# Kernel optimization log

Measured on AMD Instinct MI355X. Metric: run time of the kernel, lower is better.

## Reference

```python
import jax, jax.numpy as jnp
import numpy as np

B, C_IN, C_OUT, H, W, K = 8, 32, 32, 96, 96, 5


def setup_inputs() -> dict:
    key = jax.random.key(0)
    k1, k2 = jax.random.split(key)
    f = jax.random.normal(k1, (B, C_IN, H, W), dtype=jnp.float32)
    # xavier_uniform-style init for the structuring element h
    fan_in = C_IN * K * K
    fan_out = C_OUT * K * K
    bound = float(np.sqrt(6.0 / (fan_in + fan_out)))
    h = jax.random.uniform(k2, (C_OUT, C_IN, K, K), dtype=jnp.float32,
                           minval=-bound, maxval=bound)
    return {"f": f, "h": h}


def reference(f, h):
    """Morphological max-plus dilation with 'same' padding.

    out[b,o,y,x] = max_{c,i,j} f[b,c,y+i-p, x+j-p] + h[o,c,i,j]
    """
    b, c, hh, ww = f.shape
    o, _, k, _ = h.shape
    p = k // 2
    neg = -jnp.finfo(f.dtype).max / 2
    fp = jnp.pad(f, ((0, 0), (0, 0), (p, p), (p, p)), constant_values=neg)
    out = jnp.full((b, o, hh, ww), neg, dtype=f.dtype)
    for i in range(k):          # fixed small kernel loop (k*k = 25 taps)
        for j in range(k):
            sl = fp[:, :, i:i + hh, j:j + ww]              # (B, C, H, W)
            w_ij = h[:, :, i, j]                            # (O, C)
            # max-plus over input channels: (B,1,C,H,W) + (O,C,1,1)
            cand = jnp.max(sl[:, None] + w_ij[None, :, :, None, None], axis=2)
            out = jnp.maximum(out, cand)
    return out
```

## Files before the change

kernel.cpp:

```cpp
#include <hip/hip_runtime.h>


#define B_ 8
#define C_ 32
#define O_ 32
#define H_ 96
#define W_ 96
#define K_ 5
#define KK_ (K_ * K_)
#define NCP_ (C_ / 2)

#define TX_ 24
#define RT_ 8
#define CS_ 2
#define TY_ (RT_ * CS_)
#define NT_ (TX_ * TY_)
#define XR_ 4
#define OB_ 2
#define NOG_ (O_ / OB_)
#define CPG_ (NCP_ / CS_)

#define PH_ 100
#define PW_ 104
#define PLSZ_ (PH_ * PW_)
#define FPAD_BYTES ((size_t)B_ * NCP_ * PLSZ_ * 4)

#define HBLK_ 128
#define HPH_ 16
#define HPACK_DW (NOG_ * NCP_ * HBLK_)

#define SCALE_ 2048.0f
#define INVSCALE_ (1.0f / 2048.0f)
#define NEGQ_ (-30000)
#define NEGPACK_ 0x8AD08AD0u

typedef int sv8 __attribute__((ext_vector_type(8)));
typedef int sv2 __attribute__((ext_vector_type(2)));
typedef unsigned uv4 __attribute__((ext_vector_type(4)));

static __device__ __forceinline__ int q16(float v) {
    int q = __float2int_rn(v * SCALE_);
    q = (q < -32768) ? -32768 : q;
    q = (q > 32767) ? 32767 : q;
    return q;
}
static __device__ __forceinline__ unsigned packq(int lo, int hi) {
    return (unsigned)(lo & 0xffff) | ((unsigned)hi << 16);
}

static __device__ __forceinline__ void pk_addmax_s(int& acc, int fv, int hs) {
    int t;
    asm("v_pk_add_i16 %0, %1, %2" : "=v"(t) : "v"(fv), "s"(hs));
    asm("v_pk_max_i16 %0, %1, %2" : "=v"(acc) : "v"(acc), "v"(t));
}

static __device__ __forceinline__ int getwin(uv4 a, uv4 b, int d) {
    if (d == 0) return (int)a[0];
    if (d == 1) return (int)a[1];
    if (d == 2) return (int)a[2];
    if (d == 3) return (int)a[3];
    if (d == 4) return (int)b[0];
    if (d == 5) return (int)b[1];
    if (d == 6) return (int)b[2];
    return (int)b[3];
}

static __device__ __forceinline__ void compute_phase(int (&acc)[OB_][XR_],
        uv4 wa, uv4 wb, sv8 c0, sv2 c1) {
#pragma unroll
    for (int j = 0; j < K_; ++j) {
        const int h0 = (j * 2 < 8) ? c0[j * 2] : c1[j * 2 - 8];
        const int h1 = (j * 2 + 1 < 8) ? c0[j * 2 + 1] : c1[j * 2 + 1 - 8];
#pragma unroll
        for (int xx = 0; xx < XR_; ++xx) {
            int fv = getwin(wa, wb, xx + j);
            pk_addmax_s(acc[0][xx], fv, h0);
            pk_addmax_s(acc[1][xx], fv, h1);
        }
    }
}

#define HLOADM(B0, B1, HP, O0S, O1S)                                   \
    asm volatile("s_load_dwordx8 %0, %2, " O0S "\n\t"                  \
                 "s_load_dwordx2 %1, %2, " O1S                         \
                 : "=s"(B0), "=s"(B1) : "s"(HP))

#define WLOADM(SA, SB, PTR, O0S, O1S)                                  \
    asm volatile("global_load_dwordx4 %0, %2, off offset:" O0S "\n\t"  \
                 "global_load_dwordx4 %1, %2, off offset:" O1S         \
                 : "=v"(SA), "=v"(SB) : "v"(PTR))

#define PHASE(CH0, CH1, NH0, NH1, NHP, HO0, HO1, CW, NW, NPTR, WO0, WO1) \
    do {                                                                  \
        asm volatile("s_waitcnt lgkmcnt(0)" : "+s"(CH0), "+s"(CH1));      \
        HLOADM(NH0, NH1, NHP, HO0, HO1);                                  \
        WLOADM(NW[0], NW[1], NPTR, WO0, WO1);                             \
        asm volatile("s_waitcnt vmcnt(2)" : "+v"(CW[0]), "+v"(CW[1]));    \
        compute_phase(acc, CW[0], CW[1], CH0, CH1);                       \
    } while (0)

__global__ __launch_bounds__(256)
void prep_kernel(const float* __restrict__ f, const float* __restrict__ h,
                 unsigned* __restrict__ fpad, unsigned* __restrict__ hpack) {
    const int bz = blockIdx.z;
    if (bz < B_) {
        const int idx = blockIdx.x * 256 + threadIdx.x;
        const int cp = blockIdx.y;
        if (idx >= PLSZ_) return;
        const int row = idx / PW_;
        const int col = idx - row * PW_;
        const int y = row - 2;
        const int x = col - 2;
        unsigned pk = NEGPACK_;
        if ((unsigned)y < H_ && (unsigned)x < W_) {
            float v0 = f[((size_t)(bz * C_ + 2 * cp)     * H_ + y) * W_ + x];
            float v1 = f[((size_t)(bz * C_ + 2 * cp + 1) * H_ + y) * W_ + x];
            pk = packq(q16(v0), q16(v1));
        }
        fpad[(size_t)(bz * NCP_ + cp) * PLSZ_ + idx] = pk;
    } else {
        const int t = (blockIdx.y * gridDim.x + blockIdx.x) * 256 + threadIdx.x;
        if (t >= NOG_ * NCP_ * KK_ * OB_) return;
        const int og = t / (NCP_ * KK_ * OB_);
        int r  = t - og * (NCP_ * KK_ * OB_);
        const int cp = r / (KK_ * OB_);
        r -= cp * (KK_ * OB_);
        const int ij = r / OB_;
        const int o  = r - ij * OB_;
        const int p  = ij / K_;
        const int jj = ij - p * K_;
        float a0 = h[((size_t)(og * OB_ + o) * C_ + 2 * cp)     * KK_ + ij];
        float a1 = h[((size_t)(og * OB_ + o) * C_ + 2 * cp + 1) * KK_ + ij];
        hpack[(size_t)(og * NCP_ + cp) * HBLK_ + p * HPH_ + jj * OB_ + o] =
            packq(q16(a0), q16(a1));
    }
}

__global__ __launch_bounds__(NT_, 7)
void dilate_main(const unsigned* __restrict__ fpad,
                 const unsigned* __restrict__ hpack,
                 float* __restrict__ out) {
    const int tx  = threadIdx.x;
    const int ty  = threadIdx.y;
    const int ry  = ty & (RT_ - 1);
    const int g   = ty >> 3;
    const int gu  = __builtin_amdgcn_readfirstlane(g);

    const int ytile = blockIdx.x;
    const int og    = blockIdx.y;
    const int b     = blockIdx.z;
    const int y0 = ytile * RT_;
    const int o0 = og * OB_;
    const int x0 = XR_ * tx;
    const int yb = y0 + ry;

    __shared__ unsigned short comb[OB_ * XR_][RT_ * TX_];

    int acc[OB_][XR_];
#pragma unroll
    for (int o = 0; o < OB_; ++o)
#pragma unroll
        for (int xx = 0; xx < XR_; ++xx) acc[o][xx] = (int)NEGPACK_;

    const int cp0v = g * CPG_;
    const int cp0s = gu * CPG_;
    const unsigned* hpb = hpack + (size_t)(og * NCP_ + cp0s) * HBLK_;
    const unsigned* pvb = fpad + (size_t)(b * NCP_ + cp0v) * PLSZ_ + yb * PW_ + x0;

    sv8 hA0; sv2 hA1;
    sv8 hB0; sv2 hB1;
    uv4 winA[2], winB[2];

    HLOADM(hA0, hA1, hpb, "0x0", "0x20");
    WLOADM(winA[0], winA[1], pvb, "0", "16");

#pragma unroll 1
    for (int cpi = 0; cpi < CPG_; cpi += 2) {
        const unsigned* hb0 = hpb + (size_t)cpi * HBLK_;
        const unsigned* hb1 = hb0 + HBLK_;
        const unsigned* hb2 = (cpi + 2 < CPG_) ? hb1 + HBLK_ : hb1;
        const unsigned* pv0 = pvb + (size_t)cpi * PLSZ_;
        const unsigned* pv1 = pv0 + PLSZ_;
        const unsigned* pv2 = (cpi + 2 < CPG_) ? pv1 + PLSZ_ : pv1;

        PHASE(hA0,hA1, hB0,hB1, hb0, "0x40","0x60",   winA, winB, pv0, "416","432");
        PHASE(hB0,hB1, hA0,hA1, hb0, "0x80","0xa0",   winB, winA, pv0, "832","848");
        PHASE(hA0,hA1, hB0,hB1, hb0, "0xc0","0xe0",   winA, winB, pv0, "1248","1264");
        PHASE(hB0,hB1, hA0,hA1, hb0, "0x100","0x120", winB, winA, pv0, "1664","1680");
        PHASE(hA0,hA1, hB0,hB1, hb1, "0x0","0x20",    winA, winB, pv1, "0","16");
        PHASE(hB0,hB1, hA0,hA1, hb1, "0x40","0x60",   winB, winA, pv1, "416","432");
        PHASE(hA0,hA1, hB0,hB1, hb1, "0x80","0xa0",   winA, winB, pv1, "832","848");
        PHASE(hB0,hB1, hA0,hA1, hb1, "0xc0","0xe0",   winB, winA, pv1, "1248","1264");
        PHASE(hA0,hA1, hB0,hB1, hb1, "0x100","0x120", winA, winB, pv1, "1664","1680");
        PHASE(hB0,hB1, hA0,hA1, hb2, "0x0","0x20",    winB, winA, pv2, "0","16");
    }

    asm volatile("s_waitcnt vmcnt(0) lgkmcnt(0)"
                 : "+v"(winA[0]), "+v"(winA[1]), "+s"(hA0), "+s"(hA1));

    short red[OB_][XR_];
#pragma unroll
    for (int o = 0; o < OB_; ++o)
#pragma unroll
        for (int xx = 0; xx < XR_; ++xx) {
            short a = (short)(acc[o][xx] & 0xffff);
            short b2 = (short)(((unsigned)acc[o][xx]) >> 16);
            red[o][xx] = (a > b2) ? a : b2;
        }

    const int t192 = ry * TX_ + tx;
    if (g == 1) {
#pragma unroll
        for (int o = 0; o < OB_; ++o)
#pragma unroll
            for (int xx = 0; xx < XR_; ++xx)
                comb[o * XR_ + xx][t192] = (unsigned short)red[o][xx];
    }
    __syncthreads();
    if (g == 0) {
        const int y = yb;
#pragma unroll
        for (int o = 0; o < OB_; ++o) {
            float r[XR_];
#pragma unroll
            for (int xx = 0; xx < XR_; ++xx) {
                short m  = red[o][xx];
                short v0 = (short)comb[o * XR_ + xx][t192];
                m = (v0 > m) ? v0 : m;
                r[xx] = (float)m * INVSCALE_;
            }
            float4 v = make_float4(r[0], r[1], r[2], r[3]);
            *(float4*)&out[(((size_t)b * O_ + (o0 + o)) * H_ + y) * W_ + x0] = v;
        }
    }
}

__global__ __launch_bounds__(256)
void dilate_naive(const float* __restrict__ f, const float* __restrict__ h,
                  float* __restrict__ out) {
    const int idx = blockIdx.x * 256 + threadIdx.x;
    if (idx >= B_ * O_ * H_ * W_) return;
    const int x = idx % W_;
    const int y = (idx / W_) % H_;
    const int o = (idx / (W_ * H_)) % O_;
    const int b = idx / (W_ * H_ * O_);
    float m = -3.0e38f;
    for (int c = 0; c < C_; ++c)
        for (int i = 0; i < K_; ++i)
            for (int j = 0; j < K_; ++j) {
                int yy = y + i - 2, xc = x + j - 2;
                if ((unsigned)yy < H_ && (unsigned)xc < W_) {
                    float v = f[((size_t)(b * C_ + c) * H_ + yy) * W_ + xc] +
                              h[((size_t)o * C_ + c) * KK_ + i * K_ + j];
                    m = fmaxf(m, v);
                }
            }
    out[idx] = m;
}

extern "C" void kernel_launch(void* const* d_in, const int* in_sizes, int n_in,
                              void* d_out, int out_size, void* d_ws, size_t ws_size,
                              hipStream_t stream) {
    const float* f = (const float*)d_in[0];
    const float* h = (const float*)d_in[1];
    float* out = (float*)d_out;

    const size_t need = FPAD_BYTES + (size_t)HPACK_DW * 4;
    if (ws_size >= need) {
        unsigned* fpad  = (unsigned*)d_ws;
        unsigned* hpack = (unsigned*)((char*)d_ws + FPAD_BYTES);
        dim3 pgrid((PLSZ_ + 255) / 256, NCP_, B_ + 1);
        hipLaunchKernelGGL(prep_kernel, pgrid, dim3(256), 0, stream,
                           f, h, fpad, hpack);
        dim3 mgrid(H_ / RT_, NOG_, B_);
        dim3 mblock(TX_, TY_);
        hipLaunchKernelGGL(dilate_main, mgrid, mblock, 0, stream,
                           fpad, hpack, out);
    } else {
        hipLaunchKernelGGL(dilate_naive,
                           dim3((B_ * O_ * H_ * W_ + 255) / 256), dim3(256),
                           0, stream, f, h, out);
    }
}
```

Measured before the change: 134.7 us.

## Stage padded input row slabs through LDS with double buffering

Instead of each thread loading its 5-row input window straight from global memory per tap row, the block cooperatively loads a 12-row slab per channel pair into shared memory. The next slab is fetched while the current one is computed, and threads read their windows from LDS. This cuts redundant global/L2 traffic from overlapping rows across threads. In exchange it adds LDS usage, a __syncthreads per channel pair, and LDS-read latency that may hurt the 7-waves occupancy target.

```diff
diff --git a/kernel.cpp b/kernel.cpp
--- a/kernel.cpp
+++ b/kernel.cpp
@@ -31,8 +31,9 @@
 
 #define SCALE_ 2048.0f
 #define INVSCALE_ (1.0f / 2048.0f)
-#define NEGQ_ (-30000)
 #define NEGPACK_ 0x8AD08AD0u
+
+#define SLAB_UV4 320
 
 typedef int sv8 __attribute__((ext_vector_type(8)));
 typedef int sv2 __attribute__((ext_vector_type(2)));
@@ -85,18 +86,37 @@
                  "s_load_dwordx2 %1, %2, " O1S                         \
                  : "=s"(B0), "=s"(B1) : "s"(HP))
 
-#define WLOADM(SA, SB, PTR, O0S, O1S)                                  \
-    asm volatile("global_load_dwordx4 %0, %2, off offset:" O0S "\n\t"  \
-                 "global_load_dwordx4 %1, %2, off offset:" O1S         \
-                 : "=v"(SA), "=v"(SB) : "v"(PTR))
-
-#define PHASE(CH0, CH1, NH0, NH1, NHP, HO0, HO1, CW, NW, NPTR, WO0, WO1) \
+#define ROWPH(CH0, CH1, NH0, NH1, NHP, HO0, HO1, CW0, CW1, NW0, NW1, NR)  \
     do {                                                                  \
         asm volatile("s_waitcnt lgkmcnt(0)" : "+s"(CH0), "+s"(CH1));      \
         HLOADM(NH0, NH1, NHP, HO0, HO1);                                  \
-        WLOADM(NW[0], NW[1], NPTR, WO0, WO1);                             \
-        asm volatile("s_waitcnt vmcnt(2)" : "+v"(CW[0]), "+v"(CW[1]));    \
-        compute_phase(acc, CW[0], CW[1], CH0, CH1);                       \
+        NW0 = sbr[(NR) * 26 + tx];                                        \
+        NW1 = sbr[(NR) * 26 + tx + 1];                                    \
+        asm volatile("" : "+v"(NW0), "+v"(NW1));                          \
+        compute_phase(acc, CW0, CW1, CH0, CH1);                           \
+    } while (0)
+
+#define ROWPHL(CH0, CH1, NH0, NH1, NHP, HO0, HO1, CW0, CW1)               \
+    do {                                                                  \
+        asm volatile("s_waitcnt lgkmcnt(0)" : "+s"(CH0), "+s"(CH1));      \
+        HLOADM(NH0, NH1, NHP, HO0, HO1);                                  \
+        compute_phase(acc, CW0, CW1, CH0, CH1);                           \
+    } while (0)
+
+#define STAGE(T0, T1, GS)                                                   \
+    do {                                                                    \
+        asm volatile("global_load_dwordx4 %0, %1, off" : "=v"(T0) : "v"(GS)); \
+        if (gw < 2)                                                         \
+            asm volatile("global_load_dwordx4 %0, %1, off offset:1024"      \
+                         : "=v"(T1) : "v"(GS));                             \
+    } while (0)
+
+#define STWR(T0, T1, SW)                                                    \
+    do {                                                                    \
+        asm volatile("s_waitcnt vmcnt(0)" : "+v"(T0), "+v"(T1));            \
+        (SW)[stw] = T0;                                                     \
+        if (gw < 2) (SW)[stw + 64] = T1;                                    \
+        __syncthreads();                                                    \
     } while (0)
 
 __global__ __launch_bounds__(256)
@@ -146,14 +166,19 @@
     const int g   = ty >> 3;
     const int gu  = __builtin_amdgcn_readfirstlane(g);
 
+    const int tid  = ty * TX_ + tx;
+    const int lane = tid & 63;
+    const int wv   = tid >> 6;
+    const int gw   = wv - g * 3;
+
     const int ytile = blockIdx.x;
     const int og    = blockIdx.y;
     const int b     = blockIdx.z;
     const int y0 = ytile * RT_;
     const int o0 = og * OB_;
     const int x0 = XR_ * tx;
-    const int yb = y0 + ry;
-
+
+    __shared__ uv4 slab[CS_][2][SLAB_UV4];
     __shared__ unsigned short comb[OB_ * XR_][RT_ * TX_];
 
     int acc[OB_][XR_];
@@ -165,38 +190,70 @@
     const int cp0v = g * CPG_;
     const int cp0s = gu * CPG_;
     const unsigned* hpb = hpack + (size_t)(og * NCP_ + cp0s) * HBLK_;
-    const unsigned* pvb = fpad + (size_t)(b * NCP_ + cp0v) * PLSZ_ + yb * PW_ + x0;
+    const size_t bpl = (size_t)(b * NCP_ + cp0v);
+    const int lnoff = lane * 16 + gw * 2048;
+    const int stw   = gw * 128 + lane;
+
+    const uv4* sb0 = &slab[g][0][0];
+    const uv4* sb1 = &slab[g][1][0];
+    uv4* sw0 = &slab[g][0][0];
+    uv4* sw1 = &slab[g][1][0];
 
     sv8 hA0; sv2 hA1;
     sv8 hB0; sv2 hB1;
-    uv4 winA[2], winB[2];
+    uv4 wA0{}, wA1{}, wB0{}, wB1{};
 
     HLOADM(hA0, hA1, hpb, "0x0", "0x20");
-    WLOADM(winA[0], winA[1], pvb, "0", "16");
+    {
+        const char* gs = (const char*)(fpad + bpl * PLSZ_ + (size_t)(y0 * PW_))
+                         + lnoff;
+        uv4 t0{}, t1{};
+        STAGE(t0, t1, gs);
+        STWR(t0, t1, sw0);
+    }
 
 #pragma unroll 1
     for (int cpi = 0; cpi < CPG_; cpi += 2) {
         const unsigned* hb0 = hpb + (size_t)cpi * HBLK_;
         const unsigned* hb1 = hb0 + HBLK_;
         const unsigned* hb2 = (cpi + 2 < CPG_) ? hb1 + HBLK_ : hb1;
-        const unsigned* pv0 = pvb + (size_t)cpi * PLSZ_;
-        const unsigned* pv1 = pv0 + PLSZ_;
-        const unsigned* pv2 = (cpi + 2 < CPG_) ? pv1 + PLSZ_ : pv1;
-
-        PHASE(hA0,hA1, hB0,hB1, hb0, "0x40","0x60",   winA, winB, pv0, "416","432");
-        PHASE(hB0,hB1, hA0,hA1, hb0, "0x80","0xa0",   winB, winA, pv0, "832","848");
-        PHASE(hA0,hA1, hB0,hB1, hb0, "0xc0","0xe0",   winA, winB, pv0, "1248","1264");
-        PHASE(hB0,hB1, hA0,hA1, hb0, "0x100","0x120", winB, winA, pv0, "1664","1680");
-        PHASE(hA0,hA1, hB0,hB1, hb1, "0x0","0x20",    winA, winB, pv1, "0","16");
-        PHASE(hB0,hB1, hA0,hA1, hb1, "0x40","0x60",   winB, winA, pv1, "416","432");
-        PHASE(hA0,hA1, hB0,hB1, hb1, "0x80","0xa0",   winA, winB, pv1, "832","848");
-        PHASE(hB0,hB1, hA0,hA1, hb1, "0xc0","0xe0",   winB, winA, pv1, "1248","1264");
-        PHASE(hA0,hA1, hB0,hB1, hb1, "0x100","0x120", winA, winB, pv1, "1664","1680");
-        PHASE(hB0,hB1, hA0,hA1, hb2, "0x0","0x20",    winB, winA, pv2, "0","16");
-    }
-
-    asm volatile("s_waitcnt vmcnt(0) lgkmcnt(0)"
-                 : "+v"(winA[0]), "+v"(winA[1]), "+s"(hA0), "+s"(hA1));
+
+        {
+            const uv4* sbr = sb0;
+            const char* gs = (const char*)(fpad + (bpl + cpi + 1) * PLSZ_
+                                           + (size_t)(y0 * PW_)) + lnoff;
+            uv4 t0{}, t1{};
+            STAGE(t0, t1, gs);
+            wA0 = sbr[ry * 26 + tx];
+            wA1 = sbr[ry * 26 + tx + 1];
+            asm volatile("" : "+v"(wA0), "+v"(wA1));
+            ROWPH(hA0,hA1, hB0,hB1, hb0, "0x40","0x60",   wA0,wA1, wB0,wB1, ry+1);
+            ROWPH(hB0,hB1, hA0,hA1, hb0, "0x80","0xa0",   wB0,wB1, wA0,wA1, ry+2);
+            ROWPH(hA0,hA1, hB0,hB1, hb0, "0xc0","0xe0",   wA0,wA1, wB0,wB1, ry+3);
+            ROWPH(hB0,hB1, hA0,hA1, hb0, "0x100","0x120", wB0,wB1, wA0,wA1, ry+4);
+            ROWPHL(hA0,hA1, hB0,hB1, hb1, "0x0","0x20",   wA0,wA1);
+            STWR(t0, t1, sw1);
+        }
+
+        {
+            const uv4* sbr = sb1;
+            const char* gs = (const char*)(fpad + (bpl + cpi + 2) * PLSZ_
+                                           + (size_t)(y0 * PW_)) + lnoff;
+            uv4 t0{}, t1{};
+            STAGE(t0, t1, gs);
+            wA0 = sbr[ry * 26 + tx];
+            wA1 = sbr[ry * 26 + tx + 1];
+            asm volatile("" : "+v"(wA0), "+v"(wA1));
+            ROWPH(hB0,hB1, hA0,hA1, hb1, "0x40","0x60",   wA0,wA1, wB0,wB1, ry+1);
+            ROWPH(hA0,hA1, hB0,hB1, hb1, "0x80","0xa0",   wB0,wB1, wA0,wA1, ry+2);
+            ROWPH(hB0,hB1, hA0,hA1, hb1, "0xc0","0xe0",   wA0,wA1, wB0,wB1, ry+3);
+            ROWPH(hA0,hA1, hB0,hB1, hb1, "0x100","0x120", wB0,wB1, wA0,wA1, ry+4);
+            ROWPHL(hB0,hB1, hA0,hA1, hb2, "0x0","0x20",   wA0,wA1);
+            STWR(t0, t1, sw0);
+        }
+    }
+
+    asm volatile("s_waitcnt vmcnt(0) lgkmcnt(0)" : "+s"(hA0), "+s"(hA1));
 
     short red[OB_][XR_];
 #pragma unroll
@@ -218,7 +275,7 @@
     }
     __syncthreads();
     if (g == 0) {
-        const int y = yb;
+        const int y = y0 + ry;
 #pragma unroll
         for (int o = 0; o < OB_; ++o) {
             float r[XR_];
```

Result: slower. 142.3 us (+5.7%).
